# Kernel optimization log

Hardware: AMD Instinct MI355X
Metric: run time of the kernel (lower is better)

The kernel has to match this reference:

```python
import jax, jax.numpy as jnp
import numpy as np
from jax import lax

BZ, CAP, SEQ, INV = 32, 134, 144, 16
E_SP, E_FT = 1072, 64


def sage(x, e_src, e_dst, Wl, bl, Wr, n_nodes):
    # PyG SAGEConv (mean aggr): out = lin_l(mean_{j->i} x_j) + lin_r(x_i)
    # x: [B, N, F]; edges broadcast over batch
    msgs = x[:, e_src]                                   # [B, E, F] gather
    agg = jnp.zeros_like(x).at[:, e_dst].add(msgs)        # [B, N, F] scatter-add
    deg = jnp.zeros((n_nodes,), x.dtype).at[e_dst].add(1.0)
    mean = agg / jnp.clip(deg, 1.0)[None, :, None]
    return mean @ Wl + bl + x @ Wr


def setup_inputs() -> dict:
    key = jax.random.key(0)
    ks = jax.random.split(key, 16)
    s = lambda fan: 1.0 / np.sqrt(fan)
    inp = {
        'src': jax.random.normal(ks[0], (BZ, CAP, SEQ, INV), jnp.float32),
        'graph_edge_index': jax.random.randint(ks[1], (2, E_SP), 0, CAP, jnp.int32),
        'feature_edge_index': jax.random.randint(ks[2], (2, E_FT), 0, INV, jnp.int32),
        # spatial SAGEConv(in_var, in_var)
        'gcn_Wl': jax.random.uniform(ks[3], (INV, INV), jnp.float32, -s(INV), s(INV)),
        'gcn_bl': jnp.zeros((INV,), jnp.float32),
        'gcn_Wr': jax.random.uniform(ks[4], (INV, INV), jnp.float32, -s(INV), s(INV)),
        # feature SAGEConv(seq_len, seq_len)
        'fgcn_Wl': jax.random.uniform(ks[5], (SEQ, SEQ), jnp.float32, -s(SEQ), s(SEQ)),
        'fgcn_bl': jnp.zeros((SEQ,), jnp.float32),
        'fgcn_Wr': jax.random.uniform(ks[6], (SEQ, SEQ), jnp.float32, -s(SEQ), s(SEQ)),
        # Conv1d(in_var, in_var, k=3/5, no bias): OIW layout
        'conv1_w': jax.random.uniform(ks[7], (INV, INV, 3), jnp.float32, -s(INV * 3), s(INV * 3)),
        'conv2_w': jax.random.uniform(ks[8], (INV, INV, 5), jnp.float32, -s(INV * 5), s(INV * 5)),
        # Linear(3*in_var, in_var)
        'fc_w': jax.random.uniform(ks[9], (3 * INV, INV), jnp.float32, -s(3 * INV), s(3 * INV)),
        'fc_b': jnp.zeros((INV,), jnp.float32),
    }
    return inp


def reference(src, graph_edge_index, feature_edge_index, gcn_Wl, gcn_bl, gcn_Wr,
              fgcn_Wl, fgcn_bl, fgcn_Wr, conv1_w, conv2_w, fc_w, fc_b):
    bz, cap, seq, inv = src.shape
    # --- spatial GCN: nodes = turbines, features = in_var, batched over bz*seq
    x1 = src.transpose(0, 2, 1, 3).reshape(bz * seq, cap, inv)
    sp = sage(x1, graph_edge_index[0], graph_edge_index[1], gcn_Wl, gcn_bl, gcn_Wr, cap)
    spatial_fea = sp.reshape(bz, seq, cap, inv).transpose(0, 2, 1, 3)
    # --- feature GCN: nodes = variables, features = seq_len, batched over bz*cap
    x2 = src.transpose(0, 1, 3, 2).reshape(bz * cap, inv, seq)
    ft = sage(x2, feature_edge_index[0], feature_edge_index[1], fgcn_Wl, fgcn_bl, fgcn_Wr, inv)
    fea_fea = ft.reshape(bz, cap, inv, seq).transpose(0, 1, 3, 2)
    # --- temporal dual Conv1d over seq axis, channels = in_var
    x3 = src.reshape(bz * cap, seq, inv).transpose(0, 2, 1)  # [N, C, L]
    dn = ('NCH', 'OIH', 'NCH')
    c1 = lax.conv_general_dilated(x3, conv1_w, (1,), [(1, 1)], dimension_numbers=dn)
    c2 = lax.conv_general_dilated(x3, conv2_w, (1,), [(2, 2)], dimension_numbers=dn)
    temporal_fea = (c1 + c2).transpose(0, 2, 1).reshape(bz, cap, seq, inv)
    # --- concat + FC fusion + residual (dropout = identity at eval)
    com = jnp.concatenate([spatial_fea, fea_fea, temporal_fea], axis=-1)  # [..., 3*inv]
    out = com @ fc_w + fc_b
    return src + out
```

## Files before the change

kernel.cpp:

```cpp
#include <hip/hip_runtime.h>
#include <hip/hip_bf16.h>

#define BZn 32
#define CAPn 134
#define SEQn 144
#define INVn 16
#define ESP 1072
#define EFT 64


typedef __attribute__((ext_vector_type(8))) short bf16x8;
typedef __attribute__((ext_vector_type(4))) short short4v;
typedef __attribute__((ext_vector_type(4))) float f32x4;

#define MFMA(a, b, c) __builtin_amdgcn_mfma_f32_16x16x32_bf16(a, b, c, 0, 0, 0)

__device__ __forceinline__ unsigned short f2bf(float f) {
    union { float f; unsigned u; } v; v.f = f;
    unsigned r = v.u + 0x7fff + ((v.u >> 16) & 1);
    return (unsigned short)(r >> 16);
}
__device__ __forceinline__ float bf2f(unsigned short h) {
    union { unsigned u; float f; } v; v.u = ((unsigned)h) << 16;
    return v.f;
}
__device__ __forceinline__ unsigned pk2(float a, float b) {
    float2 v; v.x = a; v.y = b;
    union { __hip_bfloat162 h; unsigned u; } c;
    c.h = __float22bfloat162_rn(v);
    return c.u;
}
__device__ __forceinline__ short4v pack4(f32x4 v) {
    union { unsigned u[2]; short4v s; } r;
    r.u[0] = pk2(v[0], v[1]);
    r.u[1] = pk2(v[2], v[3]);
    return r.s;
}

__global__ __launch_bounds__(256) void prep_kernel(
    const int* __restrict__ ge, const int* __restrict__ fe,
    const float* __restrict__ Wl,  const float* __restrict__ Wr,
    const float* __restrict__ fWl, const float* __restrict__ fWr,
    const float* __restrict__ w1,  const float* __restrict__ w2,
    const float* __restrict__ fcw, const float* __restrict__ bl,
    const float* __restrict__ fcb,
    int* __restrict__ ws)
{
    int t = threadIdx.x;
    char* wsb = (char*)ws;
    unsigned short* uB     = (unsigned short*)(wsb + 5376);
    unsigned short* vB     = (unsigned short*)(wsb + 6400);
    unsigned short* spB2   = (unsigned short*)(wsb + 7424);
    float*          biasf  = (float*)(wsb + 8448);
    unsigned short* convA2 = (unsigned short*)(wsb + 8704);
    unsigned short* featB  = (unsigned short*)(wsb + 12800);

    __shared__ float wtile[32][145];

    if (blockIdx.x == 0) {
        int* g_rp  = ws;
        int* g_col = ws + 135;
        float* g_inv = (float*)(ws + 1207);
        __shared__ int cnt[CAPn], off[CAPn], fm[256];
        __shared__ float finv[16];
        for (int c0 = t; c0 < CAPn; c0 += 256) cnt[c0] = 0;
        fm[t] = 0;
        __syncthreads();
        for (int e = t; e < ESP; e += 256) atomicAdd(&cnt[ge[ESP + e]], 1);
        if (t < EFT) atomicAdd(&fm[fe[t] * 16 + fe[EFT + t]], 1);
        __syncthreads();
        if (t == 0) {
            int run = 0;
            for (int c0 = 0; c0 < CAPn; c0++) {
                off[c0] = run; g_rp[c0] = run;
                g_inv[c0] = 1.0f / fmaxf((float)cnt[c0], 1.0f);
                run += cnt[c0];
            }
            g_rp[CAPn] = run;
        }
        if (t < 16) {
            int dg = 0;
            for (int j = 0; j < 16; j++) dg += fm[j * 16 + t];
            finv[t] = 1.0f / fmaxf((float)dg, 1.0f);
        }
        __syncthreads();
        for (int c0 = t; c0 < CAPn; c0 += 256) cnt[c0] = 0;
        __syncthreads();
        for (int e = t; e < ESP; e += 256) {
            int d = ge[ESP + e];
            int p = off[d] + atomicAdd(&cnt[d], 1);
            g_col[p] = ge[e];
        }
        for (int u = t; u < 512; u += 256) {
            int l = u >> 3, j = u & 7, k = (l >> 4) * 8 + j, ip = l & 15;
            float vu = 0.f, vv = 0.f, vs = 0.f;
            if (k < 16) {
                for (int i = 0; i < 16; i++)
                    vu += (float)fm[k * 16 + i] * finv[i] * fcw[(16 + i) * 16 + ip];
                vv = fcw[(16 + k) * 16 + ip];
                for (int i = 0; i < 16; i++) vs += Wl[k * 16 + i] * fcw[i * 16 + ip];
            } else {
                for (int i = 0; i < 16; i++) vs += Wr[(k - 16) * 16 + i] * fcw[i * 16 + ip];
            }
            uB[u] = f2bf(vu); vB[u] = f2bf(vv); spB2[u] = f2bf(vs);
        }
        for (int u = t; u < 2048; u += 256) {
            int kk2 = u >> 9, l = (u >> 3) & 63, j = u & 7, q = l >> 4, o = l & 15;
            int kkp = kk2 * 2 + (q >> 1), i = (q & 1) * 8 + j;
            float v = 0.f;
            for (int o0 = 0; o0 < 16; o0++) {
                float w = (kkp < 3) ? w1[(o0 * 16 + i) * 3 + kkp]
                                    : w2[(o0 * 16 + i) * 5 + (kkp - 3)];
                v += w * fcw[(32 + o0) * 16 + o];
            }
            convA2[u] = f2bf(v);
        }
        if (t < 16) {
            float b0 = fcb[t], c0 = 0.f;
            for (int i = 0; i < 16; i++) {
                b0 += bl[i] * fcw[i * 16 + t];
                c0 += fcw[(16 + i) * 16 + t];
            }
            biasf[t] = b0; biasf[16 + t] = c0;
        }
    }

    int kk = blockIdx.x;
    for (int u = t; u < 32 * 144; u += 256) {
        int r = u / 144, s = u - r * 144;
        int k = kk * 32 + r;
        wtile[r][s] = (k < 144) ? fWl[k * 144 + s] : fWr[(k - 144) * 144 + s];
    }
    __syncthreads();
    for (int u = t; u < 4608; u += 256) {
        int n0 = u >> 9, rem = u & 511;
        int l = rem >> 3, j = rem & 7;
        featB[(kk * 9 + n0) * 512 + rem] = f2bf(wtile[(l >> 4) * 8 + j][n0 * 16 + (l & 15)]);
    }
}

__global__ __launch_bounds__(256, 5) void fused_kernel(
    const float* __restrict__ src,
    const float* __restrict__ fbl,
    const int* __restrict__ ws,
    float* __restrict__ out)
{
    const int* g_rp  = ws;
    const int* g_col = ws + 135;
    const float* g_inv = (const float*)(ws + 1207);
    const char* wsb = (const char*)ws;
    const unsigned short* uB     = (const unsigned short*)(wsb + 5376);
    const unsigned short* vB     = (const unsigned short*)(wsb + 6400);
    const unsigned short* spB2   = (const unsigned short*)(wsb + 7424);
    const float*          biasf  = (const float*)(wsb + 8448);
    const unsigned short* convA2 = (const unsigned short*)(wsb + 8704);
    const unsigned short* featB  = (const unsigned short*)(wsb + 12800);

    __shared__ __align__(16) unsigned short xs_bf[SEQn + 4][24];
    __shared__ __align__(16) unsigned short msp_bf[SEQn][24];
    __shared__ __align__(16) unsigned short uv_bf[INVn][312];
    __shared__ __align__(16) unsigned short t_bf[SEQn][24];
    __shared__ float sfbl[SEQn], sbias[16], scs[16];

    int t = threadIdx.x;
    int wave = t >> 6, lane = t & 63;
    int q = lane >> 4, ln = lane & 15;

    int xcd  = blockIdx.x & 7;
    int slot = blockIdx.x >> 3;
    int bl_  = slot / 134;
    int c    = slot - bl_ * 134;
    int b    = xcd * 4 + bl_;
    int bc   = b * CAPn + c;
    const float* srcb = src + (size_t)b * (CAPn * SEQn * INVn);
    const float* srcc = srcb + (size_t)c * (SEQn * INVn);

    bf16x8 caf[4];
    #pragma unroll
    for (int kk = 0; kk < 4; kk++)
        caf[kk] = *(const bf16x8*)(convA2 + (kk * 64 + lane) * 8);
    bf16x8 sbf = *(const bf16x8*)(spB2 + lane * 8);
    bf16x8 ubf = *(const bf16x8*)(uB + lane * 8);
    bf16x8 vbf = *(const bf16x8*)(vB + lane * 8);

    int rs = g_rp[c], re = g_rp[c + 1];
    float idg = g_inv[c];
    f32x4 m0 = {0.f,0.f,0.f,0.f}, m1 = {0.f,0.f,0.f,0.f}, m2 = {0.f,0.f,0.f,0.f};
    for (int e = rs; e < re; e++) {
        int n = g_col[e];
        const f32x4* p4 = (const f32x4*)(srcb + (size_t)n * (SEQn * INVn));
        m0 += p4[t];
        m1 += p4[t + 256];
        if (t < 64) m2 += p4[t + 512];
    }
    int s0g = t >> 2, i0g = (t & 3) * 4;
    m0 *= idg; m1 *= idg; m2 *= idg;
    *(short4v*)&msp_bf[s0g][i0g]      = pack4(m0);
    *(short4v*)&msp_bf[64 + s0g][i0g] = pack4(m1);
    if (t < 64) *(short4v*)&msp_bf[128 + s0g][i0g] = pack4(m2);

    const f32x4* s4 = (const f32x4*)srcc;
    f32x4 x0 = s4[t], x1 = s4[t + 256];
    *(short4v*)&xs_bf[s0g + 2][i0g]      = pack4(x0);
    *(short4v*)&xs_bf[64 + s0g + 2][i0g] = pack4(x1);
    if (t < 64) {
        f32x4 x2 = s4[t + 512];
        *(short4v*)&xs_bf[128 + s0g + 2][i0g] = pack4(x2);
    }
    if (t < 64) {
        int r = t >> 4, i = t & 15;
        int row = (r < 2) ? r : 144 + r;
        xs_bf[row][i] = 0;
    }
    if (t < SEQn) sfbl[t] = fbl[t];
    if (t < 16) { sbias[t] = biasf[t]; scs[t] = biasf[16 + t]; }
    __syncthreads();

    const int ust[4] = {0, 3, 5, 7}, ucn[4] = {3, 2, 2, 2};
    for (int tt = 0; tt < ucn[wave]; tt++) {
        int mt = ust[wave] + tt;
        int sl = mt * 16 + ln;
        bf16x8 a = {0,0,0,0,0,0,0,0};
        if (q < 2) a = *(const bf16x8*)&xs_bf[sl + 2][q * 8];
        f32x4 au = {0.f,0.f,0.f,0.f}, av = {0.f,0.f,0.f,0.f};
        au = MFMA(a, ubf, au);
        av = MFMA(a, vbf, av);
        *(short4v*)&uv_bf[ln][mt * 16 + q * 4]       = pack4(au);
        *(short4v*)&uv_bf[ln][144 + mt * 16 + q * 4] = pack4(av);
    }
    const int sst[4] = {0, 2, 4, 6}, scn[4] = {2, 2, 2, 3};
    f32x4 accS[3];
    for (int tt = 0; tt < scn[wave]; tt++) {
        int mt = sst[wave] + tt;
        int sl = mt * 16 + ln;
        const unsigned short* ap = (q < 2) ? &msp_bf[sl][(q & 1) * 8]
                                           : &xs_bf[sl + 2][(q & 1) * 8];
        bf16x8 a = *(const bf16x8*)ap;
        f32x4 z = {0.f,0.f,0.f,0.f};
        accS[tt] = MFMA(a, sbf, z);
    }
    __syncthreads();

    const int bst[4] = {0, 3, 5, 7}, bcn[4] = {3, 2, 2, 2};
    for (int tt = 0; tt < bcn[wave]; tt++) {
        int n0 = bst[wave] + tt;
        int sl = n0 * 16 + ln;
        f32x4 acc = {0.f,0.f,0.f,0.f};
        #pragma unroll
        for (int kk = 0; kk < 4; kk++) {
            int kkp = kk * 2 + (q >> 1);
            int off = (kkp < 3) ? (kkp - 1) : (kkp - 5);
            bf16x8 bb = *(const bf16x8*)&xs_bf[sl + 2 + off][(q & 1) * 8];
            acc = MFMA(caf[kk], bb, acc);
        }
        #pragma unroll
        for (int kk = 0; kk < 9; kk++) {
            bf16x8 a  = *(const bf16x8*)&uv_bf[ln][kk * 32 + q * 8];
            bf16x8 bb = *(const bf16x8*)(featB + ((kk * 9 + n0) * 64 + lane) * 8);
            acc = MFMA(a, bb, acc);
        }
        *(short4v*)&t_bf[sl][q * 4] = pack4(acc);
    }
    __syncthreads();

    float* outb = out + (size_t)bc * (SEQn * INVn);
    for (int tt = 0; tt < scn[wave]; tt++) {
        int mt = sst[wave] + tt;
        #pragma unroll
        for (int r = 0; r < 4; r++) {
            int s = mt * 16 + q * 4 + r;
            int idx = s * 16 + ln;
            outb[idx] = accS[tt][r] + bf2f(t_bf[s][ln]) + srcc[idx]
                      + sbias[ln] + sfbl[s] * scs[ln];
        }
    }
}

extern "C" void kernel_launch(void* const* d_in, const int* in_sizes, int n_in,
                              void* d_out, int out_size, void* d_ws, size_t ws_size,
                              hipStream_t stream)
{
    const float* src = (const float*)d_in[0];
    const int* ge = (const int*)d_in[1];
    const int* fe = (const int*)d_in[2];
    const float* Wl  = (const float*)d_in[3];
    const float* blp = (const float*)d_in[4];
    const float* Wr  = (const float*)d_in[5];
    const float* fWl = (const float*)d_in[6];
    const float* fbl = (const float*)d_in[7];
    const float* fWr = (const float*)d_in[8];
    const float* w1  = (const float*)d_in[9];
    const float* w2  = (const float*)d_in[10];
    const float* fcw = (const float*)d_in[11];
    const float* fcb = (const float*)d_in[12];
    float* out = (float*)d_out;
    int* ws = (int*)d_ws;

    hipLaunchKernelGGL(prep_kernel, dim3(9), dim3(256), 0, stream,
                       ge, fe, Wl, Wr, fWl, fWr, w1, w2, fcw, blp, fcb, ws);
    hipLaunchKernelGGL(fused_kernel, dim3(BZn * CAPn), dim3(256), 0, stream,
                       src, fbl, ws, out);
}
```

Before: 171.6 us.

## Stage prep weights in LDS, split prep blocks, and overlap gather loads

In the prep kernel, block 0 now loads all small weight tensors into shared memory once instead of reading them repeatedly from global memory. The feature-weight transpose tiles move to separate blocks, and the grid grows by one so block 0's serial work no longer also handles a tile. In the fused kernel, the block's own src row is loaded before the neighbour gather. The neighbour loop is unrolled by two with separate accumulators so more independent loads are in flight. This costs extra registers and may lower occupancy of the fused kernel.

```diff
diff --git a/kernel.cpp b/kernel.cpp
--- a/kernel.cpp
+++ b/kernel.cpp
@@ -55,14 +55,22 @@
     unsigned short* convA2 = (unsigned short*)(wsb + 8704);
     unsigned short* featB  = (unsigned short*)(wsb + 12800);
 
-    __shared__ float wtile[32][145];
-
     if (blockIdx.x == 0) {
         int* g_rp  = ws;
         int* g_col = ws + 135;
         float* g_inv = (float*)(ws + 1207);
+        __shared__ float swt[3360];
         __shared__ int cnt[CAPn], off[CAPn], fm[256];
         __shared__ float finv[16];
+
+        for (int u = t; u < 768;  u += 256) swt[u]        = fcw[u];
+        for (int u = t; u < 768;  u += 256) swt[768 + u]  = w1[u];
+        for (int u = t; u < 1280; u += 256) swt[1536 + u] = w2[u];
+        if (t < 256) swt[2816 + t] = Wl[t];
+        if (t < 256) swt[3072 + t] = Wr[t];
+        if (t < 16) swt[3328 + t] = bl[t];
+        if (t < 16) swt[3344 + t] = fcb[t];
+
         for (int c0 = t; c0 < CAPn; c0 += 256) cnt[c0] = 0;
         fm[t] = 0;
         __syncthreads();
@@ -96,11 +104,11 @@
             float vu = 0.f, vv = 0.f, vs = 0.f;
             if (k < 16) {
                 for (int i = 0; i < 16; i++)
-                    vu += (float)fm[k * 16 + i] * finv[i] * fcw[(16 + i) * 16 + ip];
-                vv = fcw[(16 + k) * 16 + ip];
-                for (int i = 0; i < 16; i++) vs += Wl[k * 16 + i] * fcw[i * 16 + ip];
+                    vu += (float)fm[k * 16 + i] * finv[i] * swt[(16 + i) * 16 + ip];
+                vv = swt[(16 + k) * 16 + ip];
+                for (int i = 0; i < 16; i++) vs += swt[2816 + k * 16 + i] * swt[i * 16 + ip];
             } else {
-                for (int i = 0; i < 16; i++) vs += Wr[(k - 16) * 16 + i] * fcw[i * 16 + ip];
+                for (int i = 0; i < 16; i++) vs += swt[3072 + (k - 16) * 16 + i] * swt[i * 16 + ip];
             }
             uB[u] = f2bf(vu); vB[u] = f2bf(vv); spB2[u] = f2bf(vs);
         }
@@ -109,33 +117,35 @@
             int kkp = kk2 * 2 + (q >> 1), i = (q & 1) * 8 + j;
             float v = 0.f;
             for (int o0 = 0; o0 < 16; o0++) {
-                float w = (kkp < 3) ? w1[(o0 * 16 + i) * 3 + kkp]
-                                    : w2[(o0 * 16 + i) * 5 + (kkp - 3)];
-                v += w * fcw[(32 + o0) * 16 + o];
+                float w = (kkp < 3) ? swt[768 + (o0 * 16 + i) * 3 + kkp]
+                                    : swt[1536 + (o0 * 16 + i) * 5 + (kkp - 3)];
+                v += w * swt[(32 + o0) * 16 + o];
             }
             convA2[u] = f2bf(v);
         }
         if (t < 16) {
-            float b0 = fcb[t], c0 = 0.f;
+            float b0 = swt[3344 + t], c0 = 0.f;
             for (int i = 0; i < 16; i++) {
-                b0 += bl[i] * fcw[i * 16 + t];
-                c0 += fcw[(16 + i) * 16 + t];
+                b0 += swt[3328 + i] * swt[i * 16 + t];
+                c0 += swt[(16 + i) * 16 + t];
             }
             biasf[t] = b0; biasf[16 + t] = c0;
         }
-    }
-
-    int kk = blockIdx.x;
-    for (int u = t; u < 32 * 144; u += 256) {
-        int r = u / 144, s = u - r * 144;
-        int k = kk * 32 + r;
-        wtile[r][s] = (k < 144) ? fWl[k * 144 + s] : fWr[(k - 144) * 144 + s];
-    }
-    __syncthreads();
-    for (int u = t; u < 4608; u += 256) {
-        int n0 = u >> 9, rem = u & 511;
-        int l = rem >> 3, j = rem & 7;
-        featB[(kk * 9 + n0) * 512 + rem] = f2bf(wtile[(l >> 4) * 8 + j][n0 * 16 + (l & 15)]);
+    } else {
+        __shared__ float wtile[32][145];
+        int kk = blockIdx.x - 1;
+        for (int u = t; u < 32 * 144; u += 256) {
+            int r = u / 144, s = u - r * 144;
+            int k = kk * 32 + r;
+            wtile[r][s] = (k < 144) ? fWl[k * 144 + s] : fWr[(k - 144) * 144 + s];
+        }
+        __syncthreads();
+        for (int u = t; u < 4608; u += 256) {
+            int n0 = u >> 9, rem = u & 511;
+            int l = rem >> 3, j = rem & 7;
+            featB[(kk * 9 + n0) * 512 + rem] =
+                f2bf(wtile[(l >> 4) * 8 + j][n0 * 16 + (l & 15)]);
+        }
     }
 }
 
@@ -175,6 +185,11 @@
     const float* srcb = src + (size_t)b * (CAPn * SEQn * INVn);
     const float* srcc = srcb + (size_t)c * (SEQn * INVn);
 
+    const f32x4* s4 = (const f32x4*)srcc;
+    f32x4 x0 = s4[t], x1 = s4[t + 256];
+    f32x4 x2 = {0.f,0.f,0.f,0.f};
+    if (t < 64) x2 = s4[t + 512];
+
     bf16x8 caf[4];
     #pragma unroll
     for (int kk = 0; kk < 4; kk++)
@@ -185,28 +200,32 @@
 
     int rs = g_rp[c], re = g_rp[c + 1];
     float idg = g_inv[c];
-    f32x4 m0 = {0.f,0.f,0.f,0.f}, m1 = {0.f,0.f,0.f,0.f}, m2 = {0.f,0.f,0.f,0.f};
-    for (int e = rs; e < re; e++) {
-        int n = g_col[e];
-        const f32x4* p4 = (const f32x4*)(srcb + (size_t)n * (SEQn * INVn));
-        m0 += p4[t];
-        m1 += p4[t + 256];
-        if (t < 64) m2 += p4[t + 512];
+    f32x4 m0a = {0.f,0.f,0.f,0.f}, m1a = {0.f,0.f,0.f,0.f}, m2a = {0.f,0.f,0.f,0.f};
+    f32x4 m0b = {0.f,0.f,0.f,0.f}, m1b = {0.f,0.f,0.f,0.f}, m2b = {0.f,0.f,0.f,0.f};
+    int e = rs;
+    for (; e + 1 < re; e += 2) {
+        int na = g_col[e], nb = g_col[e + 1];
+        const f32x4* pa = (const f32x4*)(srcb + (size_t)na * (SEQn * INVn));
+        const f32x4* pb = (const f32x4*)(srcb + (size_t)nb * (SEQn * INVn));
+        m0a += pa[t];       m0b += pb[t];
+        m1a += pa[t + 256]; m1b += pb[t + 256];
+        if (t < 64) { m2a += pa[t + 512]; m2b += pb[t + 512]; }
+    }
+    if (e < re) {
+        int na = g_col[e];
+        const f32x4* pa = (const f32x4*)(srcb + (size_t)na * (SEQn * INVn));
+        m0a += pa[t]; m1a += pa[t + 256];
+        if (t < 64) m2a += pa[t + 512];
     }
     int s0g = t >> 2, i0g = (t & 3) * 4;
-    m0 *= idg; m1 *= idg; m2 *= idg;
+    f32x4 m0 = (m0a + m0b) * idg, m1 = (m1a + m1b) * idg, m2 = (m2a + m2b) * idg;
     *(short4v*)&msp_bf[s0g][i0g]      = pack4(m0);
     *(short4v*)&msp_bf[64 + s0g][i0g] = pack4(m1);
     if (t < 64) *(short4v*)&msp_bf[128 + s0g][i0g] = pack4(m2);
 
-    const f32x4* s4 = (const f32x4*)srcc;
-    f32x4 x0 = s4[t], x1 = s4[t + 256];
     *(short4v*)&xs_bf[s0g + 2][i0g]      = pack4(x0);
     *(short4v*)&xs_bf[64 + s0g + 2][i0g] = pack4(x1);
-    if (t < 64) {
-        f32x4 x2 = s4[t + 512];
-        *(short4v*)&xs_bf[128 + s0g + 2][i0g] = pack4(x2);
-    }
+    if (t < 64) *(short4v*)&xs_bf[128 + s0g + 2][i0g] = pack4(x2);
     if (t < 64) {
         int r = t >> 4, i = t & 15;
         int row = (r < 2) ? r : 144 + r;
@@ -296,7 +315,7 @@
     float* out = (float*)d_out;
     int* ws = (int*)d_ws;
 
-    hipLaunchKernelGGL(prep_kernel, dim3(9), dim3(256), 0, stream,
+    hipLaunchKernelGGL(prep_kernel, dim3(10), dim3(256), 0, stream,
                        ge, fe, Wl, Wr, fWl, fWr, w1, w2, fcw, blp, fcb, ws);
     hipLaunchKernelGGL(fused_kernel, dim3(BZn * CAPn), dim3(256), 0, stream,
                        src, fbl, ws, out);
```

Result: faster. 164.9 us (-3.9%).
